# Kernel tuning notes

Hardware: AMD Instinct MI355X
Metric: run time of the kernel (lower is better)

## Reference

```python
import jax, jax.numpy as jnp
import numpy as np

EPS = 1e-5
T_THRESH = 0.0039


def layernorm2d(x, w, b):
    # normalize over channel dim (axis=1), learned affine per channel
    mu = jnp.mean(x, axis=1, keepdims=True)
    var = jnp.var(x, axis=1, keepdims=True)
    xn = (x - mu) * jax.lax.rsqrt(var + EPS)
    return xn * w[None, :, None, None] + b[None, :, None, None]


def conv1x1(x, w, b):
    # w: [O, C] (1x1 conv kernel squeezed), b: [O]
    return jnp.einsum('bchw,oc->bohw', x, w) + b[None, :, None, None]


def setup_inputs() -> dict:
    key = jax.random.key(0)
    ks = jax.random.split(key, 12)
    B, C, H, W = 8, 192, 96, 256
    s = 0.02
    inp = {
        'x_l': jax.random.normal(ks[0], (B, C, H, W), jnp.float32),
        'x_r': jax.random.normal(ks[1], (B, C, H, W), jnp.float32),
        'ln1_w': jnp.ones((C,), jnp.float32),
        'ln1_b': jnp.zeros((C,), jnp.float32),
        'ln2_w': jnp.ones((C,), jnp.float32),
        'ln2_b': jnp.zeros((C,), jnp.float32),
        'w1': jax.random.normal(ks[2], (C, C), jnp.float32) * s,
        'b1': jnp.zeros((C,), jnp.float32),
        'w2': jax.random.normal(ks[3], (C, C), jnp.float32) * s,
        'b2': jnp.zeros((C,), jnp.float32),
        'w3': jax.random.normal(ks[4], (C, C), jnp.float32) * s,
        'b3': jnp.zeros((C,), jnp.float32),
        'w4': jax.random.normal(ks[5], (C, C), jnp.float32) * s,
        'b4': jnp.zeros((C,), jnp.float32),
        'alpha': jax.random.normal(ks[6], (1, C, 1, 1), jnp.float32) * 0.1,
        'beta': jax.random.normal(ks[7], (1, C, 1, 1), jnp.float32) * 0.1,
    }
    return inp


def reference(x_l, x_r, ln1_w, ln1_b, ln2_w, ln2_b, w1, b1, w2, b2, w3, b3, w4, b4, alpha, beta):
    C = x_l.shape[1]
    scale = C ** (-0.5)
    F_u = conv1x1(layernorm2d(x_l, ln1_w, ln1_b), w1, b1)  # [B,C,H,Wl]
    F_v = conv1x1(layernorm2d(x_r, ln2_w, ln2_b), w2, b2)  # [B,C,H,Wr]
    # per-row cross attention along width: S [B,H,Wl,Wr]
    S = jnp.einsum('bchw,bchv->bhwv', F_u, F_v) * scale
    M_r2l = jax.nn.softmax(S, axis=-1)                       # [B,H,Wl,Wr]
    M_l2r = jax.nn.softmax(S.transpose(0, 1, 3, 2), axis=-1)  # [B,H,Wr,Wl]
    Vl = conv1x1(x_l, w3, b3)  # [B,C,H,Wl]
    Vr = conv1x1(x_r, w4, b4)  # [B,C,H,Wr]
    F_l2r = jnp.einsum('bhvw,bchw->bchv', M_l2r, Vl)  # [B,C,H,Wr]
    F_r2l = jnp.einsum('bhwv,bchv->bchw', M_r2l, Vr)  # [B,C,H,Wl]
    m_l2r = jnp.mean(M_l2r, axis=-1)[:, None]  # [B,1,H,Wr]
    m_r2l = jnp.mean(M_r2l, axis=-1)[:, None]  # [B,1,H,Wl]
    V_l2r = (m_l2r > T_THRESH).astype(x_l.dtype)
    V_r2l = (m_r2l > T_THRESH).astype(x_r.dtype)
    F_l = F_l2r * V_l2r * alpha
    F_r = F_r2l * V_r2l * beta
    return (x_l + F_l, x_r + F_r)
```

## Files before the change

### kernel.cpp

```cpp
#include <hip/hip_runtime.h>
#include <cstdint>
#include <cstddef>

#define C_DIM 192
#define H_DIM 96
#define W_DIM 256
#define B_DIM 8
#define ROWS (B_DIM * H_DIM)
#define HW (H_DIM * W_DIM)
#define CHW ((size_t)C_DIM * HW)
#define NE_ELEMS ((size_t)ROWS * W_DIM * C_DIM)
#define LN_EPS 1e-5f
#define ENC 63.75f
#define DEC (1.0f / 63.75f)

using u16 = unsigned short;
using u8 = unsigned char;
using f32x4 = __attribute__((ext_vector_type(4))) float;
using s16x8 = __attribute__((ext_vector_type(8))) short;

__device__ __forceinline__ float bf2f(u16 u) {
    union { unsigned int i; float f; } x; x.i = ((unsigned int)u) << 16; return x.f;
}
__device__ __forceinline__ u16 f2bf(float f) {
    union { float f; unsigned int i; } x; x.f = f;
    unsigned int r = (x.i + 0x7FFFu + ((x.i >> 16) & 1u)) >> 16;
    return (u16)r;
}
__device__ __forceinline__ float ldx(const void* p, size_t i, int isbf) {
    return isbf ? bf2f(((const u16*)p)[i]) : ((const float*)p)[i];
}
__device__ __forceinline__ void stx(void* p, size_t i, int isbf, float v) {
    if (isbf) ((u16*)p)[i] = f2bf(v); else ((float*)p)[i] = v;
}

__global__ __launch_bounds__(64) void detect_kernel(const unsigned int* __restrict__ x, int* __restrict__ flag) {
    __shared__ int cnt;
    if (threadIdx.x == 0) cnt = 0;
    __syncthreads();
    int c = 0;
    for (int i = threadIdx.x; i < 1024; i += 64) {
        unsigned int e = (x[i] >> 7) & 0xFF;
        if (e >= 100 && e <= 150) ++c;
    }
    atomicAdd(&cnt, c);
    __syncthreads();
    if (threadIdx.x == 0) *flag = (cnt > 700) ? 1 : 0;
}

__global__ __launch_bounds__(192) void prep_kernel(
    const void* __restrict__ w1, const void* __restrict__ ln1w, const void* __restrict__ ln1b, const void* __restrict__ b1,
    const void* __restrict__ w2, const void* __restrict__ ln2w, const void* __restrict__ ln2b, const void* __restrict__ b2,
    const void* __restrict__ w3, const void* __restrict__ b3, const void* __restrict__ w4, const void* __restrict__ b4,
    const void* __restrict__ alpha, const void* __restrict__ beta,
    u16* __restrict__ W1p, u16* __restrict__ W2p, u16* __restrict__ W3p, u16* __restrict__ W4p,
    float* __restrict__ rs1, float* __restrict__ c1, float* __restrict__ rs2, float* __restrict__ c2,
    float* __restrict__ b3f, float* __restrict__ b4f, float* __restrict__ alf, float* __restrict__ bef,
    const int* __restrict__ flagp)
{
    int isbf = *flagp;
    int side = blockIdx.x;
    int o = threadIdx.x;
    if (side >= 2) {
        const void* W = side == 2 ? w3 : w4;
        u16* Wp = side == 2 ? W3p : W4p;
        for (int c = 0; c < C_DIM; ++c) Wp[o * C_DIM + c] = f2bf(ldx(W, o * C_DIM + c, isbf));
        if (side == 2) { b3f[o] = ldx(b3, o, isbf); alf[o] = ldx(alpha, o, isbf); }
        else           { b4f[o] = ldx(b4, o, isbf); bef[o] = ldx(beta, o, isbf); }
        return;
    }
    const void* W  = side ? w2 : w1;
    const void* lw = side ? ln2w : ln1w;
    const void* lb = side ? ln2b : ln1b;
    const void* bb = side ? b2 : b1;
    u16* Wp   = side ? W2p : W1p;
    float* rs = side ? rs2 : rs1;
    float* cs = side ? c2 : c1;
    float f = side ? 1.0f : (0.07216878364870323f * 1.4426950408889634f);
    float rsum = 0.f, csum = 0.f;
    for (int c = 0; c < C_DIM; ++c) {
        float wv = ldx(W, o * C_DIM + c, isbf);
        u16 wb = f2bf(wv * ldx(lw, c, isbf) * f);
        Wp[o * C_DIM + c] = wb;
        rsum += bf2f(wb);
        csum += wv * ldx(lb, c, isbf);
    }
    rs[o] = rsum;
    cs[o] = f * (csum + ldx(bb, o, isbf));
}

__global__ __launch_bounds__(512, 4) void conv_kernel(
    const void* __restrict__ xl, const void* __restrict__ xr,
    const u16* __restrict__ W1p, const u16* __restrict__ W2p,
    const u16* __restrict__ W3p, const u16* __restrict__ W4p,
    const float* __restrict__ rs1, const float* __restrict__ c1,
    const float* __restrict__ rs2, const float* __restrict__ c2,
    const float* __restrict__ b3f, const float* __restrict__ b4f,
    u16* __restrict__ Fu, u16* __restrict__ Fv, u16* __restrict__ Vl, u16* __restrict__ Vr,
    const int* __restrict__ flagp)
{
    int isbf = *flagp;
    int side = blockIdx.x >> 1;
    int wblk = blockIdx.x & 1;
    int row  = blockIdx.y;
    int b = row / H_DIM, h = row - b * H_DIM;

    __shared__ u16 As[C_DIM * 40];
    __shared__ u16 Bs[128 * 40];
    __shared__ float stats[2 * 128];
    __shared__ float red[2 * 512];

    int tid = threadIdx.x;
    int lane = tid & 63, l16 = lane & 15, lq = lane >> 4;
    int wave = tid >> 6, wm = wave >> 1, wn = wave & 1;
    int m0 = wm * 48, n0 = wn * 64;

    const u16* Wp = side == 0 ? W1p : side == 1 ? W2p : side == 2 ? W3p : W4p;
    const void* xp = (side == 0 || side == 2) ? xl : xr;
    size_t xoff = (size_t)b * CHW + (size_t)h * W_DIM + wblk * 128;
    bool isLN = (side < 2);

    if (isLN) {
        int p = tid & 127, g = tid >> 7;
        float s = 0.f, s2 = 0.f;
        if (isbf) {
            const u16* xb = (const u16*)xp + xoff;
            for (int c = g; c < C_DIM; c += 4) { float v = bf2f(xb[(size_t)c * HW + p]); s += v; s2 += v * v; }
        } else {
            const float* xf = (const float*)xp + xoff;
            for (int c = g; c < C_DIM; c += 4) { float v = xf[(size_t)c * HW + p]; s += v; s2 += v * v; }
        }
        red[tid] = s; red[512 + tid] = s2;
    }
    __syncthreads();
    if (isLN && tid < 128) {
        float s  = red[tid] + red[tid + 128] + red[tid + 256] + red[tid + 384];
        float s2 = red[512 + tid] + red[512 + tid + 128] + red[512 + tid + 256] + red[512 + tid + 384];
        float mu = s * (1.f / C_DIM);
        float var = s2 * (1.f / C_DIM) - mu * mu;
        stats[tid] = mu;
        stats[128 + tid] = rsqrtf(var + LN_EPS);
    }
    __syncthreads();

    f32x4 acc[3][4];
    f32x4 zz = {0.f, 0.f, 0.f, 0.f};
    #pragma unroll
    for (int i = 0; i < 3; ++i)
        #pragma unroll
        for (int j = 0; j < 4; ++j) acc[i][j] = zz;

    for (int kk = 0; kk < 6; ++kk) {
        int k0 = kk * 32;
        for (int i = tid; i < C_DIM * 4; i += 512) {
            int r = i >> 2, q = i & 3;
            *(uint4*)&As[r * 40 + q * 8] = *(const uint4*)(Wp + r * C_DIM + k0 + q * 8);
        }
        {
            int r = tid >> 4, sg = tid & 15;
            size_t base = xoff + (size_t)(k0 + r) * HW + sg * 8;
            u16 tmp[8];
            if (isbf) {
                union { uint4 v; u16 us[8]; } t;
                t.v = *(const uint4*)((const u16*)xp + base);
                #pragma unroll
                for (int j = 0; j < 8; ++j) tmp[j] = t.us[j];
            } else {
                const float* xf = (const float*)xp + base;
                #pragma unroll
                for (int j = 0; j < 8; ++j) tmp[j] = f2bf(xf[j]);
            }
            #pragma unroll
            for (int j = 0; j < 8; ++j) Bs[(sg * 8 + j) * 40 + r] = tmp[j];
        }
        __syncthreads();
        s16x8 a[3], bfr[4];
        #pragma unroll
        for (int tm = 0; tm < 3; ++tm) a[tm] = *(const s16x8*)&As[(m0 + tm * 16 + l16) * 40 + lq * 8];
        #pragma unroll
        for (int tn = 0; tn < 4; ++tn) bfr[tn] = *(const s16x8*)&Bs[(n0 + tn * 16 + l16) * 40 + lq * 8];
        #pragma unroll
        for (int tm = 0; tm < 3; ++tm)
            #pragma unroll
            for (int tn = 0; tn < 4; ++tn)
                acc[tm][tn] = __builtin_amdgcn_mfma_f32_16x16x32_bf16(a[tm], bfr[tn], acc[tm][tn], 0, 0, 0);
        __syncthreads();
    }

    const float* rs = side == 0 ? rs1 : rs2;
    const float* cs = side == 0 ? c1 : c2;
    const float* bias = side == 2 ? b3f : b4f;
    u16* outp = side == 0 ? Fu : side == 1 ? Fv : side == 2 ? Vl : Vr;

    #pragma unroll
    for (int tm = 0; tm < 3; ++tm) {
        #pragma unroll
        for (int tn = 0; tn < 4; ++tn) {
            int p = n0 + tn * 16 + l16;
            #pragma unroll
            for (int r = 0; r < 4; ++r) {
                int o = m0 + tm * 16 + lq * 4 + r;
                float v = acc[tm][tn][r];
                if (isLN) {
                    v = stats[128 + p] * (v - stats[p] * rs[o]) + cs[o];
                    outp[((size_t)row * W_DIM + wblk * 128 + p) * C_DIM + o] = f2bf(v);
                } else {
                    v += bias[o];
                    outp[((size_t)row * C_DIM + o) * W_DIM + wblk * 128 + p] = f2bf(v);
                }
            }
        }
    }
}

__global__ __launch_bounds__(512, 4) void score_kernel(
    const u16* __restrict__ Fu, const u16* __restrict__ Fv, u8* __restrict__ E)
{
    int whalf = blockIdx.x;
    int row = blockIdx.y;
    __shared__ u16 As[128 * 40];
    __shared__ u16 Bs[256 * 40];
    int tid = threadIdx.x, lane = tid & 63, l16 = lane & 15, lq = lane >> 4;
    int wave = tid >> 6, wm = wave >> 2, wn = wave & 3;
    int m0 = wm * 64, n0 = wn * 64;

    f32x4 acc[4][4];
    f32x4 zz = {0.f, 0.f, 0.f, 0.f};
    #pragma unroll
    for (int i = 0; i < 4; ++i)
        #pragma unroll
        for (int j = 0; j < 4; ++j) acc[i][j] = zz;

    const u16* Abase = Fu + ((size_t)row * W_DIM + whalf * 128) * C_DIM;
    const u16* Bbase = Fv + (size_t)row * W_DIM * C_DIM;

    for (int kk = 0; kk < 6; ++kk) {
        int k0 = kk * 32;
        {
            int r = tid >> 2, q = tid & 3;
            *(uint4*)&As[r * 40 + q * 8] = *(const uint4*)(Abase + (size_t)r * C_DIM + k0 + q * 8);
        }
        for (int i = tid; i < 256 * 4; i += 512) {
            int r = i >> 2, q = i & 3;
            *(uint4*)&Bs[r * 40 + q * 8] = *(const uint4*)(Bbase + (size_t)r * C_DIM + k0 + q * 8);
        }
        __syncthreads();
        s16x8 a[4], bfr[4];
        #pragma unroll
        for (int tm = 0; tm < 4; ++tm) a[tm] = *(const s16x8*)&As[(m0 + tm * 16 + l16) * 40 + lq * 8];
        #pragma unroll
        for (int tn = 0; tn < 4; ++tn) bfr[tn] = *(const s16x8*)&Bs[(n0 + tn * 16 + l16) * 40 + lq * 8];
        #pragma unroll
        for (int tm = 0; tm < 4; ++tm)
            #pragma unroll
            for (int tn = 0; tn < 4; ++tn)
                acc[tm][tn] = __builtin_amdgcn_mfma_f32_16x16x32_bf16(a[tm], bfr[tn], acc[tm][tn], 0, 0, 0);
        __syncthreads();
    }

    u8* Ebase = E + ((size_t)row * W_DIM + whalf * 128) * W_DIM;
    #pragma unroll
    for (int tm = 0; tm < 4; ++tm) {
        #pragma unroll
        for (int tn = 0; tn < 4; ++tn) {
            int v = n0 + tn * 16 + l16;
            #pragma unroll
            for (int r = 0; r < 4; ++r) {
                int wl = m0 + tm * 16 + lq * 4 + r;
                float e = exp2f(acc[tm][tn][r]);
                e = fminf(e, 4.0f);
                int q = (int)(e * ENC + 0.5f);
                Ebase[(size_t)wl * W_DIM + v] = (u8)(q > 255 ? 255 : q);
            }
        }
    }
}

__global__ __launch_bounds__(512, 4) void apply_kernel(
    const u8* __restrict__ E, const u16* __restrict__ Vl, const u16* __restrict__ Vr,
    const void* __restrict__ xl, const void* __restrict__ xr,
    const float* __restrict__ alf, const float* __restrict__ bef,
    void* __restrict__ out,
    const int* __restrict__ flagp)
{
    int isbf = *flagp;
    int half = blockIdx.x;
    int row = blockIdx.y;
    int b = row / H_DIM, h = row - b * H_DIM;

    __shared__ u16 Vs[C_DIM * 40];
    __shared__ u16 Es[128 * 40];
    __shared__ float red[512];
    __shared__ float dnm[128];

    int tid = threadIdx.x, lane = tid & 63, l16 = lane & 15, lq = lane >> 4;
    int wave = tid >> 6, wm = wave >> 1, wn = wave & 1;
    int m0 = wm * 48, n0 = wn * 64;
    f32x4 zz = {0.f, 0.f, 0.f, 0.f};

    f32x4 acc[3][4];
    #pragma unroll
    for (int i = 0; i < 3; ++i)
        #pragma unroll
        for (int j = 0; j < 4; ++j) acc[i][j] = zz;
    float psum = 0.f;

    const u8* Eb2 = E + ((size_t)row * W_DIM + half * 128) * W_DIM;
    const u16* Vrb = Vr + (size_t)row * C_DIM * W_DIM;

    for (int kk = 0; kk < 8; ++kk) {
        int v0 = kk * 32;
        for (int i = tid; i < C_DIM * 4; i += 512) {
            int r = i >> 2, q = i & 3;
            *(uint4*)&Vs[r * 40 + q * 8] = *(const uint4*)(Vrb + (size_t)r * W_DIM + v0 + q * 8);
        }
        {
            int r = tid >> 2, q = tid & 3;
            union { uint2 v; u8 c[8]; } t;
            t.v = *(const uint2*)(Eb2 + (size_t)r * W_DIM + v0 + q * 8);
            #pragma unroll
            for (int j = 0; j < 8; ++j) Es[r * 40 + q * 8 + j] = f2bf((float)t.c[j] * DEC);
        }
        __syncthreads();
        {
            int w = tid & 127, g = tid >> 7;
            float s = 0.f;
            #pragma unroll
            for (int j = 0; j < 8; ++j) s += bf2f(Es[w * 40 + g * 8 + j]);
            psum += s;
        }
        s16x8 a[3], bfr[4];
        #pragma unroll
        for (int tm = 0; tm < 3; ++tm) a[tm] = *(const s16x8*)&Vs[(m0 + tm * 16 + l16) * 40 + lq * 8];
        #pragma unroll
        for (int tn = 0; tn < 4; ++tn) bfr[tn] = *(const s16x8*)&Es[(n0 + tn * 16 + l16) * 40 + lq * 8];
        #pragma unroll
        for (int tm = 0; tm < 3; ++tm)
            #pragma unroll
            for (int tn = 0; tn < 4; ++tn)
                acc[tm][tn] = __builtin_amdgcn_mfma_f32_16x16x32_bf16(a[tm], bfr[tn], acc[tm][tn], 0, 0, 0);
        __syncthreads();
    }
    red[tid] = psum;
    __syncthreads();
    if (tid < 128) dnm[tid] = red[tid] + red[tid + 128] + red[tid + 256] + red[tid + 384];
    __syncthreads();

    #pragma unroll
    for (int tm = 0; tm < 3; ++tm) {
        #pragma unroll
        for (int tn = 0; tn < 4; ++tn) {
            int wl = n0 + tn * 16 + l16;
            int w = half * 128 + wl;
            #pragma unroll
            for (int r = 0; r < 4; ++r) {
                int c_o = m0 + tm * 16 + lq * 4 + r;
                size_t xi = ((size_t)(b * C_DIM + c_o) * H_DIM + h) * W_DIM + w;
                float v = acc[tm][tn][r] / dnm[wl] * bef[c_o] + ldx(xr, xi, isbf);
                stx(out, NE_ELEMS + xi, isbf, v);
            }
        }
    }
    __syncthreads();

    #pragma unroll
    for (int i = 0; i < 3; ++i)
        #pragma unroll
        for (int j = 0; j < 4; ++j) acc[i][j] = zz;
    psum = 0.f;
    const u16* Vlb = Vl + (size_t)row * C_DIM * W_DIM;

    for (int kk = 0; kk < 8; ++kk) {
        int w0 = kk * 32;
        for (int i = tid; i < C_DIM * 4; i += 512) {
            int r = i >> 2, q = i & 3;
            *(uint4*)&Vs[r * 40 + q * 8] = *(const uint4*)(Vlb + (size_t)r * W_DIM + w0 + q * 8);
        }
        {
            int r = tid >> 4, sg = tid & 15;
            union { uint2 v; u8 c[8]; } t;
            t.v = *(const uint2*)(E + ((size_t)row * W_DIM + w0 + r) * W_DIM + half * 128 + sg * 8);
            #pragma unroll
            for (int j = 0; j < 8; ++j) Es[(sg * 8 + j) * 40 + r] = f2bf((float)t.c[j] * DEC);
        }
        __syncthreads();
        {
            int vv = tid & 127, g = tid >> 7;
            float s = 0.f;
            #pragma unroll
            for (int j = 0; j < 8; ++j) s += bf2f(Es[vv * 40 + g * 8 + j]);
            psum += s;
        }
        s16x8 a[3], bfr[4];
        #pragma unroll
        for (int tm = 0; tm < 3; ++tm) a[tm] = *(const s16x8*)&Vs[(m0 + tm * 16 + l16) * 40 + lq * 8];
        #pragma unroll
        for (int tn = 0; tn < 4; ++tn) bfr[tn] = *(const s16x8*)&Es[(n0 + tn * 16 + l16) * 40 + lq * 8];
        #pragma unroll
        for (int tm = 0; tm < 3; ++tm)
            #pragma unroll
            for (int tn = 0; tn < 4; ++tn)
                acc[tm][tn] = __builtin_amdgcn_mfma_f32_16x16x32_bf16(a[tm], bfr[tn], acc[tm][tn], 0, 0, 0);
        __syncthreads();
    }
    red[tid] = psum;
    __syncthreads();
    if (tid < 128) dnm[tid] = red[tid] + red[tid + 128] + red[tid + 256] + red[tid + 384];
    __syncthreads();

    #pragma unroll
    for (int tm = 0; tm < 3; ++tm) {
        #pragma unroll
        for (int tn = 0; tn < 4; ++tn) {
            int vl = n0 + tn * 16 + l16;
            int v = half * 128 + vl;
            #pragma unroll
            for (int r = 0; r < 4; ++r) {
                int c_o = m0 + tm * 16 + lq * 4 + r;
                size_t xi = ((size_t)(b * C_DIM + c_o) * H_DIM + h) * W_DIM + v;
                float val = acc[tm][tn][r] / dnm[vl] * alf[c_o] + ldx(xl, xi, isbf);
                stx(out, xi, isbf, val);
            }
        }
    }
}

extern "C" void kernel_launch(void* const* d_in, const int* in_sizes, int n_in,
                              void* d_out, int out_size, void* d_ws, size_t ws_size,
                              hipStream_t stream)
{
    const void* xl   = d_in[0];
    const void* xr   = d_in[1];
    const void* ln1w = d_in[2];
    const void* ln1b = d_in[3];
    const void* ln2w = d_in[4];
    const void* ln2b = d_in[5];
    const void* w1   = d_in[6];
    const void* b1   = d_in[7];
    const void* w2   = d_in[8];
    const void* b2   = d_in[9];
    const void* w3   = d_in[10];
    const void* b3   = d_in[11];
    const void* w4   = d_in[12];
    const void* b4   = d_in[13];
    const void* alpha = d_in[14];
    const void* beta  = d_in[15];

    size_t NE  = NE_ELEMS;
    size_t NEe = (size_t)ROWS * W_DIM * W_DIM;
    u16* Fu = (u16*)d_ws;
    u16* Fv = Fu + NE;
    u16* Vl = Fv + NE;
    u16* Vr = Vl + NE;
    u8*  Eq = (u8*)(Vr + NE);
    u16* W1p = (u16*)(Eq + NEe);
    u16* W2p = W1p + C_DIM * C_DIM;
    u16* W3p = W2p + C_DIM * C_DIM;
    u16* W4p = W3p + C_DIM * C_DIM;
    float* rs1 = (float*)(W4p + C_DIM * C_DIM);
    float* c1  = rs1 + C_DIM;
    float* rs2 = c1 + C_DIM;
    float* c2  = rs2 + C_DIM;
    float* b3f = c2 + C_DIM;
    float* b4f = b3f + C_DIM;
    float* alf = b4f + C_DIM;
    float* bef = alf + C_DIM;
    int* flag  = (int*)(bef + C_DIM);

    hipLaunchKernelGGL(detect_kernel, dim3(1), dim3(64), 0, stream, (const unsigned int*)xl, flag);
    hipLaunchKernelGGL(prep_kernel, dim3(4), dim3(192), 0, stream,
                       w1, ln1w, ln1b, b1, w2, ln2w, ln2b, b2, w3, b3, w4, b4, alpha, beta,
                       W1p, W2p, W3p, W4p, rs1, c1, rs2, c2, b3f, b4f, alf, bef, flag);
    hipLaunchKernelGGL(conv_kernel, dim3(8, ROWS), dim3(512), 0, stream,
                       xl, xr, W1p, W2p, W3p, W4p, rs1, c1, rs2, c2, b3f, b4f, Fu, Fv, Vl, Vr, flag);
    hipLaunchKernelGGL(score_kernel, dim3(2, ROWS), dim3(512), 0, stream, Fu, Fv, Eq);
    hipLaunchKernelGGL(apply_kernel, dim3(2, ROWS), dim3(512), 0, stream,
                       Eq, Vl, Vr, xl, xr, alf, bef, d_out, flag);
}
```

Before: 1.554 ms.

## Fuse LayerNorm stats into GEMM tile loads and vectorize shared-memory stores

Drops the separate pass that reads the whole input channel column for LayerNorm statistics. The sums are now accumulated while the GEMM B-tile is loaded, and mean and rstd are finalized after the K loop. Tile loads are remapped so each thread gathers 8 channel values for one pixel and writes them to shared memory as a single 16-byte store instead of 8 scattered u16 stores. The attention-weight row sums are also computed in registers during the E tile staging, which removes an extra LDS read pass. In exchange, global loads become per-element strided gathers rather than vector loads.

```diff
diff --git a/kernel.cpp b/kernel.cpp
--- a/kernel.cpp
+++ b/kernel.cpp
@@ -120,35 +120,15 @@
     size_t xoff = (size_t)b * CHW + (size_t)h * W_DIM + wblk * 128;
     bool isLN = (side < 2);
 
-    if (isLN) {
-        int p = tid & 127, g = tid >> 7;
-        float s = 0.f, s2 = 0.f;
-        if (isbf) {
-            const u16* xb = (const u16*)xp + xoff;
-            for (int c = g; c < C_DIM; c += 4) { float v = bf2f(xb[(size_t)c * HW + p]); s += v; s2 += v * v; }
-        } else {
-            const float* xf = (const float*)xp + xoff;
-            for (int c = g; c < C_DIM; c += 4) { float v = xf[(size_t)c * HW + p]; s += v; s2 += v * v; }
-        }
-        red[tid] = s; red[512 + tid] = s2;
-    }
-    __syncthreads();
-    if (isLN && tid < 128) {
-        float s  = red[tid] + red[tid + 128] + red[tid + 256] + red[tid + 384];
-        float s2 = red[512 + tid] + red[512 + tid + 128] + red[512 + tid + 256] + red[512 + tid + 384];
-        float mu = s * (1.f / C_DIM);
-        float var = s2 * (1.f / C_DIM) - mu * mu;
-        stats[tid] = mu;
-        stats[128 + tid] = rsqrtf(var + LN_EPS);
-    }
-    __syncthreads();
-
     f32x4 acc[3][4];
     f32x4 zz = {0.f, 0.f, 0.f, 0.f};
     #pragma unroll
     for (int i = 0; i < 3; ++i)
         #pragma unroll
         for (int j = 0; j < 4; ++j) acc[i][j] = zz;
+
+    float s_ln = 0.f, s2_ln = 0.f;
+    int wv = tid & 127, g = tid >> 7;
 
     for (int kk = 0; kk < 6; ++kk) {
         int k0 = kk * 32;
@@ -157,21 +137,24 @@
             *(uint4*)&As[r * 40 + q * 8] = *(const uint4*)(Wp + r * C_DIM + k0 + q * 8);
         }
         {
-            int r = tid >> 4, sg = tid & 15;
-            size_t base = xoff + (size_t)(k0 + r) * HW + sg * 8;
-            u16 tmp[8];
+            size_t base = xoff + (size_t)(k0 + g * 8) * HW + wv;
+            float v8[8];
             if (isbf) {
-                union { uint4 v; u16 us[8]; } t;
-                t.v = *(const uint4*)((const u16*)xp + base);
+                const u16* xb = (const u16*)xp;
                 #pragma unroll
-                for (int j = 0; j < 8; ++j) tmp[j] = t.us[j];
+                for (int j = 0; j < 8; ++j) v8[j] = bf2f(xb[base + (size_t)j * HW]);
             } else {
-                const float* xf = (const float*)xp + base;
+                const float* xf = (const float*)xp;
                 #pragma unroll
-                for (int j = 0; j < 8; ++j) tmp[j] = f2bf(xf[j]);
-            }
-            #pragma unroll
-            for (int j = 0; j < 8; ++j) Bs[(sg * 8 + j) * 40 + r] = tmp[j];
+                for (int j = 0; j < 8; ++j) v8[j] = xf[base + (size_t)j * HW];
+            }
+            union { s16x8 v; u16 us[8]; } pk;
+            #pragma unroll
+            for (int j = 0; j < 8; ++j) {
+                if (isLN) { s_ln += v8[j]; s2_ln += v8[j] * v8[j]; }
+                pk.us[j] = f2bf(v8[j]);
+            }
+            *(s16x8*)&Bs[wv * 40 + g * 8] = pk.v;
         }
         __syncthreads();
         s16x8 a[3], bfr[4];
@@ -184,6 +167,20 @@
             #pragma unroll
             for (int tn = 0; tn < 4; ++tn)
                 acc[tm][tn] = __builtin_amdgcn_mfma_f32_16x16x32_bf16(a[tm], bfr[tn], acc[tm][tn], 0, 0, 0);
+        __syncthreads();
+    }
+
+    if (isLN) {
+        red[tid] = s_ln; red[512 + tid] = s2_ln;
+        __syncthreads();
+        if (tid < 128) {
+            float s  = red[tid] + red[tid + 128] + red[tid + 256] + red[tid + 384];
+            float s2 = red[512 + tid] + red[512 + tid + 128] + red[512 + tid + 256] + red[512 + tid + 384];
+            float mu = s * (1.f / C_DIM);
+            float var = s2 * (1.f / C_DIM) - mu * mu;
+            stats[tid] = mu;
+            stats[128 + tid] = rsqrtf(var + LN_EPS);
+        }
         __syncthreads();
     }
 
@@ -318,17 +315,16 @@
             int r = tid >> 2, q = tid & 3;
             union { uint2 v; u8 c[8]; } t;
             t.v = *(const uint2*)(Eb2 + (size_t)r * W_DIM + v0 + q * 8);
-            #pragma unroll
-            for (int j = 0; j < 8; ++j) Es[r * 40 + q * 8 + j] = f2bf((float)t.c[j] * DEC);
-        }
-        __syncthreads();
-        {
-            int w = tid & 127, g = tid >> 7;
-            float s = 0.f;
-            #pragma unroll
-            for (int j = 0; j < 8; ++j) s += bf2f(Es[w * 40 + g * 8 + j]);
-            psum += s;
-        }
+            union { s16x8 v; u16 us[8]; } pk;
+            #pragma unroll
+            for (int j = 0; j < 8; ++j) {
+                u16 bw = f2bf((float)t.c[j] * DEC);
+                pk.us[j] = bw;
+                psum += bf2f(bw);
+            }
+            *(s16x8*)&Es[r * 40 + q * 8] = pk.v;
+        }
+        __syncthreads();
         s16x8 a[3], bfr[4];
         #pragma unroll
         for (int tm = 0; tm < 3; ++tm) a[tm] = *(const s16x8*)&Vs[(m0 + tm * 16 + l16) * 40 + lq * 8];
@@ -343,7 +339,7 @@
     }
     red[tid] = psum;
     __syncthreads();
-    if (tid < 128) dnm[tid] = red[tid] + red[tid + 128] + red[tid + 256] + red[tid + 384];
+    if (tid < 128) dnm[tid] = red[4 * tid] + red[4 * tid + 1] + red[4 * tid + 2] + red[4 * tid + 3];
     __syncthreads();
 
     #pragma unroll
@@ -370,6 +366,8 @@
     psum = 0.f;
     const u16* Vlb = Vl + (size_t)row * C_DIM * W_DIM;
 
+    int vv = tid & 127, g = tid >> 7;
+
     for (int kk = 0; kk < 8; ++kk) {
         int w0 = kk * 32;
         for (int i = tid; i < C_DIM * 4; i += 512) {
@@ -377,20 +375,17 @@
             *(uint4*)&Vs[r * 40 + q * 8] = *(const uint4*)(Vlb + (size_t)r * W_DIM + w0 + q * 8);
         }
         {
-            int r = tid >> 4, sg = tid & 15;
-            union { uint2 v; u8 c[8]; } t;
-            t.v = *(const uint2*)(E + ((size_t)row * W_DIM + w0 + r) * W_DIM + half * 128 + sg * 8);
-            #pragma unroll
-            for (int j = 0; j < 8; ++j) Es[(sg * 8 + j) * 40 + r] = f2bf((float)t.c[j] * DEC);
-        }
-        __syncthreads();
-        {
-            int vv = tid & 127, g = tid >> 7;
-            float s = 0.f;
-            #pragma unroll
-            for (int j = 0; j < 8; ++j) s += bf2f(Es[vv * 40 + g * 8 + j]);
-            psum += s;
-        }
+            const u8* Ep = E + ((size_t)row * W_DIM + w0 + g * 8) * W_DIM + half * 128 + vv;
+            union { s16x8 v; u16 us[8]; } pk;
+            #pragma unroll
+            for (int j = 0; j < 8; ++j) {
+                u16 bw = f2bf((float)Ep[(size_t)j * W_DIM] * DEC);
+                pk.us[j] = bw;
+                psum += bf2f(bw);
+            }
+            *(s16x8*)&Es[vv * 40 + g * 8] = pk.v;
+        }
+        __syncthreads();
         s16x8 a[3], bfr[4];
         #pragma unroll
         for (int tm = 0; tm < 3; ++tm) a[tm] = *(const s16x8*)&Vs[(m0 + tm * 16 + l16) * 40 + lq * 8];
```

Measured after the change: 1.312 ms. 15.6% less time.
